# Optimization experiments

Hardware: AMD Instinct MI355X
Metric: run time of the kernel (lower is better)

Reference implementation:

```python
import jax, jax.numpy as jnp
import numpy as np

LN_EPS = 1e-5
NEG_INF = -1e30


def setup_inputs() -> dict:
    key = jax.random.key(0)
    k_adj, k_feat, k_mask, k_w = jax.random.split(key, 4)
    B, N, H, R, L = 8, 400, 768, 46, 2
    adj = jax.random.uniform(k_adj, (B, N, N, R), dtype=jnp.float32)
    feature = jax.random.normal(k_feat, (B, N, H), dtype=jnp.float32)
    dmask = (jax.random.uniform(k_mask, (B, 1, N)) > 0.1).astype(jnp.float32)
    # per-layer, per-relation Linear(H, H, bias=False) weights, applied as x @ W
    W = jax.random.normal(k_w, (L, R, H, H), dtype=jnp.float32) / np.sqrt(H)
    return {"adj": adj, "feature": feature, "dmask": dmask, "W": W}


def reference(adj, feature, dmask, W):
    # adj: [B,N,N,R] -> [B,R,N,N]; dmask: [B,1,N] masks key/column axis
    B, N, _, R = adj.shape
    a = jnp.transpose(adj, (0, 3, 1, 2))           # [B,R,N,N]
    m = dmask[:, None, :, :]                        # [B,1,1,N]
    logits = a * m + (1.0 - m) * NEG_INF
    att = jax.nn.softmax(logits, axis=-1)           # [B,R,N,N] (layer-invariant)

    x = feature
    num_layers = W.shape[0]
    for layer in range(num_layers):
        # grouped per-relation linear: h[b,r,n,k] = feature[b,n,h] @ W[layer,r,h,k]
        h = jnp.einsum('bnh,rhk->brnk', x, W[layer])
        h = jax.nn.relu(jnp.einsum('brnm,brmk->brnk', att, h))
        addition = h.sum(axis=1)                    # sum over relations -> [B,N,H]
        z = jax.nn.relu(addition) / R
        # LayerNorm without affine params
        mu = jnp.mean(z, axis=-1, keepdims=True)
        var = jnp.var(z, axis=-1, keepdims=True)
        x = (z - mu) / jnp.sqrt(var + LN_EPS)
        # dropout is identity in eval mode
    return x
```

## Files before the change

### kernel.cpp

```cpp
#include <hip/hip_runtime.h>
#include <stdint.h>

#define BS 8
#define NN 400
#define HH 768
#define RR 46
#define MB 416
#define APAD 448
#define MFLAT2 3328
#define LDW2 3328

typedef _Float16 half8 __attribute__((ext_vector_type(8)));
typedef _Float16 half4v __attribute__((ext_vector_type(4)));
typedef float floatx4 __attribute__((ext_vector_type(4)));

__device__ __forceinline__ void async16(const void* g, void* l) {
  __builtin_amdgcn_global_load_lds((const __attribute__((address_space(1))) uint32_t*)g,
                                   (__attribute__((address_space(3))) uint32_t*)l, 16, 0, 0);
}

__device__ __forceinline__ int xcd_work(int flat, int nwg) {
  int q = nwg >> 3, rem = nwg & 7;
  int xcd = flat & 7, slot = flat >> 3;
  return (xcd < rem ? xcd * (q + 1) : rem * (q + 1) + (xcd - rem) * q) + slot;
}

__device__ __forceinline__ void vm_waitN(int n) {
  if (n >= 4) asm volatile("s_waitcnt vmcnt(4)" ::: "memory");
  else if (n == 3) asm volatile("s_waitcnt vmcnt(3)" ::: "memory");
  else if (n == 2) asm volatile("s_waitcnt vmcnt(2)" ::: "memory");
  else if (n == 1) asm volatile("s_waitcnt vmcnt(1)" ::: "memory");
  else asm volatile("s_waitcnt vmcnt(0)" ::: "memory");
}
#define BAR_ONE() { asm volatile("s_barrier" ::: "memory"); __builtin_amdgcn_sched_barrier(0); }


__device__ __forceinline__ void mma_tiles(const _Float16* As, const _Float16* Bs, int lane,
                                          int wr, int wc, floatx4 acc[4][4]) {
  int arow = wr + (lane & 15);
  int brow = wc + (lane & 15);
  int kswz = ((lane >> 4) ^ ((lane >> 1) & 3)) * 8;
  half8 a[4], b[4];
#pragma unroll
  for (int i = 0; i < 4; ++i) a[i] = *(const half8*)&As[(arow + i * 16) * 32 + kswz];
#pragma unroll
  for (int i = 0; i < 4; ++i) b[i] = *(const half8*)&Bs[(brow + i * 16) * 32 + kswz];
#pragma unroll
  for (int i = 0; i < 4; ++i)
#pragma unroll
    for (int j = 0; j < 4; ++j)
      acc[i][j] = __builtin_amdgcn_mfma_f32_16x16x32_f16(a[i], b[j], acc[i][j], 0, 0, 0);
}

__device__ __forceinline__ void mma16b(const _Float16* As, const _Float16* Bs, int lane,
                                       int wr, int wc, floatx4 acc[8][2]) {
  int arow = wr + (lane & 15);
  int brow = wc + (lane & 15);
  int kswz = ((lane >> 4) ^ ((lane >> 1) & 3)) * 8;
  half8 a[8], b[2];
#pragma unroll
  for (int i = 0; i < 8; ++i) a[i] = *(const half8*)&As[(arow + i * 16) * 32 + kswz];
#pragma unroll
  for (int j = 0; j < 2; ++j) b[j] = *(const half8*)&Bs[(brow + j * 16) * 32 + kswz];
#pragma unroll
  for (int i = 0; i < 8; ++i)
#pragma unroll
    for (int j = 0; j < 2; ++j)
      acc[i][j] = __builtin_amdgcn_mfma_f32_16x16x32_f16(a[i], b[j], acc[i][j], 0, 0, 0);
}

__global__ __launch_bounds__(256) void conv_w(const float* __restrict__ W, _Float16* __restrict__ Wt) {
  __shared__ float tl[32][33];
  int t = threadIdx.x;
  int lr = blockIdx.y;
  int tr = blockIdx.x / 24, tc = blockIdx.x % 24;
  const float* src = W + (size_t)lr * HH * HH;
  _Float16* dst = Wt + (size_t)lr * HH * HH;
  int rl = t >> 5, cl = t & 31;
#pragma unroll
  for (int j = 0; j < 4; ++j)
    tl[rl + 8 * j][cl] = src[(size_t)(tr * 32 + rl + 8 * j) * HH + tc * 32 + cl];
  __syncthreads();
#pragma unroll
  for (int j = 0; j < 4; ++j)
    dst[(size_t)(tc * 32 + rl + 8 * j) * HH + tr * 32 + cl] = (_Float16)tl[cl][rl + 8 * j];
}

__global__ void conv_x(const float* __restrict__ f, _Float16* __restrict__ x16) {
  int i4 = blockIdx.x * 256 + threadIdx.x;
  int row = i4 / 192;
  int c4 = i4 - row * 192;
  int b = row / 416;
  int m = row - b * 416;
  half4v h = {};
  if (m < NN) {
    float4 v = *(const float4*)(f + ((size_t)(b * NN + m) * HH) + c4 * 4);
    h[0] = (_Float16)v.x; h[1] = (_Float16)v.y; h[2] = (_Float16)v.z; h[3] = (_Float16)v.w;
  }
  *(half4v*)&x16[(size_t)row * HH + c4 * 4] = h;
}

__global__ __launch_bounds__(512) void att_softmax(const float* __restrict__ adj,
                                                   const float* __restrict__ dmask,
                                                   _Float16* __restrict__ att) {
  __shared__ _Float16 sE[NN * RR];
  __shared__ float sM[NN];
  int t = threadIdx.x;
  int n = blockIdx.x, b = blockIdx.y;
  const float4* src = (const float4*)(adj + ((size_t)b * NN + n) * NN * RR);
  for (int i = t; i < NN; i += 512) sM[i] = dmask[b * NN + i];
  float4 v[9];
#pragma unroll
  for (int k = 0; k < 9; ++k) {
    int idx = t + k * 512;
    if (idx < NN * RR / 4) v[k] = src[idx];
  }
#pragma unroll
  for (int k = 0; k < 9; ++k) {
    int idx = t + k * 512;
    if (idx < NN * RR / 4) {
      half4v h;
      h[0] = (_Float16)__expf(v[k].x);
      h[1] = (_Float16)__expf(v[k].y);
      h[2] = (_Float16)__expf(v[k].z);
      h[3] = (_Float16)__expf(v[k].w);
      *(half4v*)&sE[idx * 4] = h;
    }
  }
  __syncthreads();
  int lane = t & 63, wid = t >> 6;
  for (int r = wid; r < RR; r += 8) {
    float s = 0.f;
    for (int m = lane; m < NN; m += 64)
      if (sM[m] > 0.5f) s += (float)sE[m * RR + r];
#pragma unroll
    for (int o = 32; o; o >>= 1) s += __shfl_xor(s, o);
    float inv = 1.0f / s;
    _Float16* orow = att + (((size_t)b * RR + r) * NN + n) * APAD;
    for (int m4 = lane * 4; m4 < APAD; m4 += 256) {
      half4v o = {};
#pragma unroll
      for (int e = 0; e < 4; ++e) {
        int m = m4 + e;
        if (m < NN && sM[m] > 0.5f) o[e] = (_Float16)((float)sE[m * RR + r] * inv);
      }
      *(half4v*)&orow[m4] = o;
    }
  }
}

__global__ __launch_bounds__(512, 4) void gemm_xw(const _Float16* __restrict__ x16,
                                                  const _Float16* __restrict__ Wt,
                                                  _Float16* __restrict__ h1T, int layer, int r0, int rbase) {
  extern __shared__ __align__(16) char smraw[];
  int t = threadIdx.x;
  int work = xcd_work(blockIdx.x, gridDim.x);
  int r_i = work / 78;
  int rem = work - r_i * 78;
  int r = r0 + r_i;
  int mtile = rem / 6, ntile = rem % 6;
  const _Float16* Bp = Wt + ((size_t)layer * RR + r) * HH * HH;
  int lane = t & 63, w = t >> 6;
  int wr = (w >> 2) * 128, wc = (w & 3) * 32;
  floatx4 acc[8][2] = {};

  int swz = ((lane & 3) ^ ((lane >> 3) & 3)) * 8;
  int ga0 = mtile * 256 + w * 32 + (lane >> 2);
  int ga1 = ga0 + 16;
  int gb = ntile * 128 + w * 16 + (lane >> 2);
  const _Float16* pa0 = x16 + (size_t)ga0 * HH + swz;
  const _Float16* pa1 = x16 + (size_t)ga1 * HH + swz;
  const _Float16* pb = Bp + (size_t)gb * HH + swz;
  auto issue = [&](int buf) {
    _Float16* lA = (_Float16*)(smraw + buf * 24576) + (w * 2) * 512;
    _Float16* lB = (_Float16*)(smraw + buf * 24576 + 16384) + w * 512;
    async16(pa0, lA); async16(pa1, lA + 512);
    async16(pb, lB);
    pa0 += 32; pa1 += 32; pb += 32;
  };

  issue(0); issue(1);
  asm volatile("s_waitcnt vmcnt(3)" ::: "memory");
  BAR_ONE();
  int cur = 0, nxt = 2;
  for (int s = 0; s < 24; ++s) {
    if (s + 2 < 24) { issue(nxt); nxt = nxt == 2 ? 0 : nxt + 1; }
    char* cb = smraw + cur * 24576;
    __builtin_amdgcn_s_setprio(1);
    mma16b((const _Float16*)cb, (const _Float16*)(cb + 16384), lane, wr, wc, acc);
    __builtin_amdgcn_s_setprio(0);
    if (s + 1 < 24) {
      if (s + 2 < 24) { asm volatile("s_waitcnt vmcnt(3)" ::: "memory"); }
      else            { asm volatile("s_waitcnt vmcnt(0)" ::: "memory"); }
      BAR_ONE();
    }
    cur = cur == 2 ? 0 : cur + 1;
  }
  __syncthreads();

  _Float16* outl = (_Float16*)smraw + (size_t)w * 4096;
#pragma unroll
  for (int i = 0; i < 8; ++i) {
#pragma unroll
    for (int j = 0; j < 2; ++j) {
      int rl = i * 16 + (lane >> 4) * 4;
      int cl = j * 16 + (lane & 15);
      int pos = rl ^ ((cl & 7) << 3);
      half4v v = {(_Float16)acc[i][j][0], (_Float16)acc[i][j][1],
                  (_Float16)acc[i][j][2], (_Float16)acc[i][j][3]};
      *(half4v*)&outl[cl * 128 + pos] = v;
    }
  }
  _Float16* outp = h1T + (size_t)(r - rbase) * HH * LDW2;
  int gmb = mtile * 256 + wr;
  int gnb = ntile * 128 + wc;
#pragma unroll
  for (int p = 0; p < 8; ++p) {
    int c = p * 4 + (lane >> 4);
    int mq = (lane & 15) * 8;
    int mpos = mq ^ ((c & 7) << 3);
    half8 v = *(const half8*)&outl[c * 128 + mpos];
    *(half8*)&outp[(size_t)(gnb + c) * LDW2 + gmb + mq] = v;
  }
}

__global__ __launch_bounds__(512, 2) void gemm_att(const _Float16* __restrict__ att,
                                                   const _Float16* __restrict__ h1T,
                                                   float* __restrict__ partials, size_t psz,
                                                   int rs, int rcount, int rbase, int accflag,
                                                   int ngroups) {
  extern __shared__ __align__(16) char smraw[];
  int t = threadIdx.x;
  int work = xcd_work(blockIdx.x, gridDim.x);
  int ntile = work % 6;
  int tmp = work / 6;
  int mtile = tmp & 1; tmp >>= 1;
  int g = tmp % ngroups;
  int b = tmp / ngroups;
  int rbeg = rs + (g * rcount) / ngroups;
  int rend = rs + ((g + 1) * rcount) / ngroups;
  int nr = rend - rbeg;
  int total = nr * 13;
  float* part = partials + (size_t)g * psz;
  int lane = t & 63, w = t >> 6;
  int wr = (w >> 1) * 64, wc = (w & 1) * 64;
  floatx4 acc[4][4] = {}, sum[4][4] = {};

  int swz = ((lane & 3) ^ ((lane >> 3) & 3)) * 8;
  int ga0 = mtile * 256 + w * 32 + (lane >> 2);
  int ga1 = ga0 + 16;
  ga0 = ga0 > NN - 1 ? NN - 1 : ga0;
  ga1 = ga1 > NN - 1 ? NN - 1 : ga1;
  int gb = ntile * 128 + w * 16 + (lane >> 2);
  const _Float16* pa0 = att + ((size_t)b * RR + rbeg) * NN * APAD + (size_t)ga0 * APAD + swz;
  const _Float16* pa1 = att + ((size_t)b * RR + rbeg) * NN * APAD + (size_t)ga1 * APAD + swz;
  const _Float16* pb = h1T + (size_t)(rbeg - rbase) * HH * LDW2 + (size_t)gb * LDW2 + b * MB + swz;
  int nskA = 0, nskB = 0;
  auto issueA = [&](int k) {
    _Float16* lA = (_Float16*)(smraw + (k % 3) * 16384) + (w * 2) * 512;
    async16(pa0, lA); async16(pa1, lA + 512);
    if (++nskA == 13) { nskA = 0; pa0 += (size_t)NN * APAD - 384; pa1 += (size_t)NN * APAD - 384; }
    else { pa0 += 32; pa1 += 32; }
  };
  auto issueB = [&](int k) {
    _Float16* lB = (_Float16*)(smraw + 49152 + (k % 6) * 8192) + w * 512;
    async16(pb, lB);
    if (++nskB == 13) { nskB = 0; pb += (size_t)HH * LDW2 - 384; }
    else { pb += 32; }
  };

  issueA(0);
  issueB(0); issueB(1); issueB(2); issueB(3); issueB(4);
  issueA(1);
  asm volatile("s_waitcnt vmcnt(6)" ::: "memory");
  BAR_ONE();
  int cks = 0;
  for (int s = 0; s < total; ++s) {
    if (s + 2 < total) issueA(s + 2);
    if (s + 5 < total) issueB(s + 5);
    const _Float16* As = (const _Float16*)(smraw + (s % 3) * 16384);
    const _Float16* Bs = (const _Float16*)(smraw + 49152 + (s % 6) * 8192);
    __builtin_amdgcn_s_setprio(1);
    mma_tiles(As, Bs, lane, wr, wc, acc);
    __builtin_amdgcn_s_setprio(0);
    if (cks == 12) {
#pragma unroll
      for (int i = 0; i < 4; ++i)
#pragma unroll
        for (int j = 0; j < 4; ++j) {
#pragma unroll
          for (int q2 = 0; q2 < 4; ++q2) sum[i][j][q2] += fmaxf(acc[i][j][q2], 0.0f);
          acc[i][j] = (floatx4){0.f, 0.f, 0.f, 0.f};
        }
      cks = 0;
    } else ++cks;
    if (s + 1 < total) {
      int N = (s == 0) ? 3
                       : ((s + 4 < total ? 1 : 0) + (s + 2 < total ? 2 : 0) + (s + 5 < total ? 1 : 0));
      vm_waitN(N);
      BAR_ONE();
    }
  }
#pragma unroll
  for (int i = 0; i < 4; ++i) {
    int rl = wr + i * 16 + (lane >> 4) * 4;
    int grow = mtile * 256 + rl;
#pragma unroll
    for (int j = 0; j < 4; ++j) {
      int gcol = ntile * 128 + wc + j * 16 + (lane & 15);
#pragma unroll
      for (int q2 = 0; q2 < 4; ++q2) {
        if (grow + q2 < NN) {
          size_t idx = ((size_t)b * NN + grow + q2) * HH + gcol;
          float v = sum[i][j][q2];
          if (accflag) v += part[idx];
          part[idx] = v;
        }
      }
    }
  }
}

__global__ __launch_bounds__(256) void lnorm(const float* __restrict__ partials, size_t psz, int np,
                                             _Float16* __restrict__ x16, float* __restrict__ out) {
  int row = blockIdx.x;
  int t = threadIdx.x;
  int b = row / NN;
  int xrow = row + b * 16;
  float v[3];
  float s = 0.f, s2 = 0.f;
#pragma unroll
  for (int j = 0; j < 3; ++j) {
    float a = 0.f;
    for (int gidx = 0; gidx < np; ++gidx) a += partials[(size_t)gidx * psz + (size_t)row * HH + t + j * 256];
    v[j] = fmaxf(a, 0.f) * (1.0f / RR);
    s += v[j];
    s2 += v[j] * v[j];
  }
#pragma unroll
  for (int o = 32; o; o >>= 1) {
    s += __shfl_xor(s, o);
    s2 += __shfl_xor(s2, o);
  }
  __shared__ float rs_[4], rs2_[4];
  int lane = t & 63, wid = t >> 6;
  if (!lane) { rs_[wid] = s; rs2_[wid] = s2; }
  __syncthreads();
  s = rs_[0] + rs_[1] + rs_[2] + rs_[3];
  s2 = rs2_[0] + rs2_[1] + rs2_[2] + rs2_[3];
  float mu = s * (1.0f / HH);
  float var = s2 * (1.0f / HH) - mu * mu;
  float rstd = rsqrtf(var + 1e-5f);
#pragma unroll
  for (int j = 0; j < 3; ++j) {
    float o = (v[j] - mu) * rstd;
    out[(size_t)row * HH + t + j * 256] = o;
    x16[(size_t)xrow * HH + t + j * 256] = (_Float16)o;
  }
}

extern "C" void kernel_launch(void* const* d_in, const int* in_sizes, int n_in,
                              void* d_out, int out_size, void* d_ws, size_t ws_size,
                              hipStream_t stream) {
  const float* adj = (const float*)d_in[0];
  const float* feature = (const float*)d_in[1];
  const float* dmask = (const float*)d_in[2];
  const float* W = (const float*)d_in[3];
  float* out = (float*)d_out;

  (void)hipFuncSetAttribute((const void*)gemm_xw,
                            hipFuncAttributeMaxDynamicSharedMemorySize, 73728);
  (void)hipFuncSetAttribute((const void*)gemm_att,
                            hipFuncAttributeMaxDynamicSharedMemorySize, 98304);

  uintptr_t base = (uintptr_t)d_ws;
  uintptr_t p = base;
  auto alloc = [&](size_t bytes) -> void* {
    uintptr_t q = (p + 255) & ~(uintptr_t)255;
    p = q + bytes;
    return (void*)q;
  };
  _Float16* att = (_Float16*)alloc((size_t)BS * RR * NN * APAD * 2);
  _Float16* Wt = (_Float16*)alloc((size_t)2 * RR * HH * HH * 2);
  _Float16* x16 = (_Float16*)alloc((size_t)MFLAT2 * HH * 2);
  size_t psz = (size_t)(BS * NN) * HH;
  size_t pszB = psz * 4;
  size_t used = p - base;
  size_t rem = ws_size > used ? ws_size - used : 0;
  size_t perR = (size_t)HH * LDW2 * 2;
  size_t h1full = (size_t)RR * perR;

  conv_w<<<dim3(576, 2 * RR), 256, 0, stream>>>(W, Wt);
  conv_x<<<MFLAT2 * HH / 4 / 256, 256, 0, stream>>>(feature, x16);
  att_softmax<<<dim3(NN, BS), 512, 0, stream>>>(adj, dmask, att);

  if (rem >= h1full + 4 * pszB + 512) {
    _Float16* h1T = (_Float16*)alloc(h1full);
    int ngroups = (int)(((ws_size - (p - base)) - 256) / pszB);
    if (ngroups > 8) ngroups = 8;
    float* partials = (float*)alloc((size_t)ngroups * pszB);
    for (int layer = 0; layer < 2; ++layer) {
      gemm_xw<<<78 * RR, 512, 73728, stream>>>(x16, Wt, h1T, layer, 0, 0);
      gemm_att<<<96 * ngroups, 512, 98304, stream>>>(att, h1T, partials, psz, 0, RR, 0, 0, ngroups);
      lnorm<<<BS * NN, 256, 0, stream>>>(partials, psz, ngroups, x16, out);
    }
  } else {
    float* partials = (float*)alloc(pszB);
    size_t rem2 = ws_size > (p - base) ? ws_size - (p - base) : 0;
    int RCmax = (int)(rem2 / perR);
    if (RCmax > RR) RCmax = RR;
    if (RCmax < 1) RCmax = 1;
    _Float16* h1T = (_Float16*)alloc((size_t)RCmax * perR);
    for (int layer = 0; layer < 2; ++layer) {
      for (int r0 = 0; r0 < RR; r0 += RCmax) {
        int rc = RR - r0 < RCmax ? RR - r0 : RCmax;
        gemm_xw<<<78 * rc, 512, 73728, stream>>>(x16, Wt, h1T, layer, r0, r0);
        gemm_att<<<96 * 1, 512, 98304, stream>>>(att, h1T, partials, psz, r0, rc, r0, r0 > 0, 1);
      }
      lnorm<<<BS * NN, 256, 0, stream>>>(partials, psz, 1, x16, out);
    }
  }
}
```

Baseline: 970.5 us.

## Deepen gemm_att LDS pipeline and process two k-steps per barrier

Enlarges the A-tile ring in gemm_att from 3 to 6 stages (LDS grows to 144KB) and restructures the main loop to issue loads four steps ahead and compute two k-steps between each wait/barrier pair. The goal is to halve the barrier count and keep more async global-to-LDS loads in flight, hiding memory latency. The larger LDS footprint leaves room for only one 512-thread workgroup per CU, and the wait counting becomes more involved.

```diff
diff --git a/kernel.cpp b/kernel.cpp
--- a/kernel.cpp
+++ b/kernel.cpp
@@ -26,11 +26,18 @@
 }
 
 __device__ __forceinline__ void vm_waitN(int n) {
-  if (n >= 4) asm volatile("s_waitcnt vmcnt(4)" ::: "memory");
-  else if (n == 3) asm volatile("s_waitcnt vmcnt(3)" ::: "memory");
-  else if (n == 2) asm volatile("s_waitcnt vmcnt(2)" ::: "memory");
-  else if (n == 1) asm volatile("s_waitcnt vmcnt(1)" ::: "memory");
-  else asm volatile("s_waitcnt vmcnt(0)" ::: "memory");
+  int c = n > 8 ? 8 : n;
+  switch (c) {
+    case 8: asm volatile("s_waitcnt vmcnt(8)" ::: "memory"); break;
+    case 7: asm volatile("s_waitcnt vmcnt(7)" ::: "memory"); break;
+    case 6: asm volatile("s_waitcnt vmcnt(6)" ::: "memory"); break;
+    case 5: asm volatile("s_waitcnt vmcnt(5)" ::: "memory"); break;
+    case 4: asm volatile("s_waitcnt vmcnt(4)" ::: "memory"); break;
+    case 3: asm volatile("s_waitcnt vmcnt(3)" ::: "memory"); break;
+    case 2: asm volatile("s_waitcnt vmcnt(2)" ::: "memory"); break;
+    case 1: asm volatile("s_waitcnt vmcnt(1)" ::: "memory"); break;
+    default: asm volatile("s_waitcnt vmcnt(0)" ::: "memory"); break;
+  }
 }
 #define BAR_ONE() { asm volatile("s_barrier" ::: "memory"); __builtin_amdgcn_sched_barrier(0); }
 
@@ -257,29 +264,21 @@
   const _Float16* pb = h1T + (size_t)(rbeg - rbase) * HH * LDW2 + (size_t)gb * LDW2 + b * MB + swz;
   int nskA = 0, nskB = 0;
   auto issueA = [&](int k) {
-    _Float16* lA = (_Float16*)(smraw + (k % 3) * 16384) + (w * 2) * 512;
+    _Float16* lA = (_Float16*)(smraw + (k % 6) * 16384) + (w * 2) * 512;
     async16(pa0, lA); async16(pa1, lA + 512);
     if (++nskA == 13) { nskA = 0; pa0 += (size_t)NN * APAD - 384; pa1 += (size_t)NN * APAD - 384; }
     else { pa0 += 32; pa1 += 32; }
   };
   auto issueB = [&](int k) {
-    _Float16* lB = (_Float16*)(smraw + 49152 + (k % 6) * 8192) + w * 512;
+    _Float16* lB = (_Float16*)(smraw + 98304 + (k % 6) * 8192) + w * 512;
     async16(pb, lB);
     if (++nskB == 13) { nskB = 0; pb += (size_t)HH * LDW2 - 384; }
     else { pb += 32; }
   };
-
-  issueA(0);
-  issueB(0); issueB(1); issueB(2); issueB(3); issueB(4);
-  issueA(1);
-  asm volatile("s_waitcnt vmcnt(6)" ::: "memory");
-  BAR_ONE();
   int cks = 0;
-  for (int s = 0; s < total; ++s) {
-    if (s + 2 < total) issueA(s + 2);
-    if (s + 5 < total) issueB(s + 5);
-    const _Float16* As = (const _Float16*)(smraw + (s % 3) * 16384);
-    const _Float16* Bs = (const _Float16*)(smraw + 49152 + (s % 6) * 8192);
+  auto step_compute = [&](int s) {
+    const _Float16* As = (const _Float16*)(smraw + (s % 6) * 16384);
+    const _Float16* Bs = (const _Float16*)(smraw + 98304 + (s % 6) * 8192);
     __builtin_amdgcn_s_setprio(1);
     mma_tiles(As, Bs, lane, wr, wc, acc);
     __builtin_amdgcn_s_setprio(0);
@@ -294,10 +293,33 @@
         }
       cks = 0;
     } else ++cks;
-    if (s + 1 < total) {
-      int N = (s == 0) ? 3
-                       : ((s + 4 < total ? 1 : 0) + (s + 2 < total ? 2 : 0) + (s + 5 < total ? 1 : 0));
-      vm_waitN(N);
+  };
+
+  int ni2 = 0;
+  if (0 < total) issueA(0);
+  if (1 < total) issueA(1);
+  if (0 < total) issueB(0);
+  if (1 < total) issueB(1);
+  if (2 < total) { issueA(2); ni2 += 2; }
+  if (3 < total) { issueA(3); ni2 += 2; }
+  if (2 < total) { issueB(2); ni2 += 1; }
+  if (3 < total) { issueB(3); ni2 += 1; }
+  vm_waitN(ni2);
+  BAR_ONE();
+
+  int s = 0;
+  while (s < total) {
+    int pair = (total - s >= 2) ? 2 : 1;
+    int ni = 0;
+    if (s + 4 < total) { issueA(s + 4); ni += 2; }
+    if (pair == 2 && s + 5 < total) { issueA(s + 5); ni += 2; }
+    if (s + 4 < total) { issueB(s + 4); ni += 1; }
+    if (pair == 2 && s + 5 < total) { issueB(s + 5); ni += 1; }
+    step_compute(s);
+    if (pair == 2) step_compute(s + 1);
+    s += pair;
+    if (s < total) {
+      vm_waitN(ni);
       BAR_ONE();
     }
   }
@@ -371,7 +393,7 @@
   (void)hipFuncSetAttribute((const void*)gemm_xw,
                             hipFuncAttributeMaxDynamicSharedMemorySize, 73728);
   (void)hipFuncSetAttribute((const void*)gemm_att,
-                            hipFuncAttributeMaxDynamicSharedMemorySize, 98304);
+                            hipFuncAttributeMaxDynamicSharedMemorySize, 147456);
 
   uintptr_t base = (uintptr_t)d_ws;
   uintptr_t p = base;
@@ -401,7 +423,7 @@
     float* partials = (float*)alloc((size_t)ngroups * pszB);
     for (int layer = 0; layer < 2; ++layer) {
       gemm_xw<<<78 * RR, 512, 73728, stream>>>(x16, Wt, h1T, layer, 0, 0);
-      gemm_att<<<96 * ngroups, 512, 98304, stream>>>(att, h1T, partials, psz, 0, RR, 0, 0, ngroups);
+      gemm_att<<<96 * ngroups, 512, 147456, stream>>>(att, h1T, partials, psz, 0, RR, 0, 0, ngroups);
       lnorm<<<BS * NN, 256, 0, stream>>>(partials, psz, ngroups, x16, out);
     }
   } else {
@@ -415,7 +437,7 @@
       for (int r0 = 0; r0 < RR; r0 += RCmax) {
         int rc = RR - r0 < RCmax ? RR - r0 : RCmax;
         gemm_xw<<<78 * rc, 512, 73728, stream>>>(x16, Wt, h1T, layer, r0, r0);
-        gemm_att<<<96 * 1, 512, 98304, stream>>>(att, h1T, partials, psz, r0, rc, r0, r0 > 0, 1);
+        gemm_att<<<96 * 1, 512, 147456, stream>>>(att, h1T, partials, psz, r0, rc, r0, r0 > 0, 1);
       }
       lnorm<<<BS * NN, 256, 0, stream>>>(partials, psz, 1, x16, out);
     }
```

Result: no change. 970.9 us (+0.0%).
